# Optimization experiments

Hardware: AMD Instinct MI355X
Metric: run time of the kernel (lower is better)

The kernel has to match this reference:

```python
import jax, jax.numpy as jnp
import numpy as np

N, E, D, H1, H2 = 50000, 800000, 128, 128, 128


def setup_inputs() -> dict:
    key = jax.random.key(0)
    ks = jax.random.split(key, 9)
    s = 0.05
    return {
        "x": jax.random.normal(ks[0], (N, D), dtype=jnp.float32),
        "edge_index": jax.random.randint(ks[1], (2, E), 0, N, dtype=jnp.int64),
        "W_l1": jax.random.normal(ks[2], (D, H1), dtype=jnp.float32) * s,
        "b_l1": jnp.zeros((H1,), dtype=jnp.float32),
        "W_r1": jax.random.normal(ks[3], (D, H1), dtype=jnp.float32) * s,
        "W_l2": jax.random.normal(ks[4], (H1, H2), dtype=jnp.float32) * s,
        "b_l2": jnp.zeros((H2,), dtype=jnp.float32),
        "W_r2": jax.random.normal(ks[5], (H1, H2), dtype=jnp.float32) * s,
        "W_e": jax.random.normal(ks[6], (2 * H2, 1), dtype=jnp.float32) * s,
        "b_e": jnp.zeros((1,), dtype=jnp.float32),
    }


def _sage_conv(h, src, tgt, n_nodes, W_l, b_l, W_r):
    # PyG SAGEConv (mean aggr): out = lin_l(mean_{j in N(i)} h_j) + lin_r(h_i)
    msg = h[src]                                              # [E, F] gather
    agg = jax.ops.segment_sum(msg, tgt, num_segments=n_nodes)  # [N, F]
    cnt = jax.ops.segment_sum(jnp.ones((src.shape[0], 1), h.dtype), tgt,
                              num_segments=n_nodes)            # [N, 1]
    mean = agg / jnp.maximum(cnt, 1.0)                         # empty nbrs -> 0
    return mean @ W_l + b_l + h @ W_r


def reference(x, edge_index, W_l1, b_l1, W_r1, W_l2, b_l2, W_r2, W_e, b_e):
    src, tgt = edge_index[0], edge_index[1]
    n_nodes = x.shape[0]
    h = jax.nn.relu(_sage_conv(x, src, tgt, n_nodes, W_l1, b_l1, W_r1))
    # dropout is identity in eval mode
    h = _sage_conv(h, src, tgt, n_nodes, W_l2, b_l2, W_r2)
    z = jnp.concatenate([h[src], h[tgt]], axis=-1)  # [E, 2*H2]
    y = z @ W_e + b_e                                # [E, 1]
    return jax.nn.sigmoid(y)
```

## Files before the change

### kernel.cpp

```cpp
#include <hip/hip_runtime.h>

#define NN 50000
#define NE 800000
#define DD 128
#define BUCKETS 196
#define PB 4096
#define PBLK 196
#define EMAX 6144
#define PACKB 6250
#define WTB 128

typedef unsigned int uint_t;
typedef unsigned short ush_t;
typedef __attribute__((ext_vector_type(8))) short short8;
typedef __attribute__((ext_vector_type(4))) float f32x4;

__device__ __forceinline__ float bflo(uint_t u) { return __uint_as_float(u << 16); }
__device__ __forceinline__ float bfhi(uint_t u) { return __uint_as_float(u & 0xffff0000u); }
__device__ __forceinline__ ush_t f2bf(float f) {
  uint_t u = __float_as_uint(f);
  u += 0x7fffu + ((u >> 16) & 1u);
  return (ush_t)(u >> 16);
}
__device__ __forceinline__ uint_t pack2(float a, float b) {
  return (uint_t)f2bf(a) | ((uint_t)f2bf(b) << 16);
}

__device__ __forceinline__ int ld_idx(const void* ei, int is64, long long i) {
  return is64 ? (int)((const long long*)ei)[i] : ((const int*)ei)[i];
}

__device__ __forceinline__ int detect64(const void* ei) {
  const unsigned long long* p = (const unsigned long long*)ei;
  unsigned long long w = p[threadIdx.x & 63];
  return __ballot((w >> 32) != 0) == 0ull ? 1 : 0;
}

__device__ __forceinline__ int block_incl_scan(int v, int tid, int* wsum) {
  int lane = tid & 63, wave = tid >> 6;
  int s = v;
#pragma unroll
  for (int off = 1; off < 64; off <<= 1) {
    int u = __shfl_up(s, off, 64);
    if (lane >= off) s += u;
  }
  if (lane == 63) wsum[wave] = s;
  __syncthreads();
  int base = 0;
  if (wave > 0) base += wsum[0];
  if (wave > 1) base += wsum[1];
  if (wave > 2) base += wsum[2];
  return base + s;
}

__global__ __launch_bounds__(256) void prep_part_k(
    const void* __restrict__ ei, int* __restrict__ bcur,
    uint_t* __restrict__ pbuf, uint_t* __restrict__ epk,
    const float* __restrict__ x, ush_t* __restrict__ xb,
    const float* __restrict__ Wl1, const float* __restrict__ Wr1,
    const float* __restrict__ Wl2, const float* __restrict__ Wr2,
    const float* __restrict__ We, const float* __restrict__ bl2,
    const float* __restrict__ be,
    ush_t* __restrict__ Wt1, float* __restrict__ uv, float* __restrict__ cc) {
  __shared__ int hist[256];
  __shared__ int basel[256];
  __shared__ int cur[256];
  __shared__ int gbase[256];
  __shared__ int wsum[4];
  __shared__ uint_t buf[PB];
  __shared__ unsigned char bbuf[PB];
  int tid = threadIdx.x;
  int blk = blockIdx.x;
  if (blk >= PBLK) {
    int blk2 = blk - PBLK;
    if (blk2 < 2) {
      const float* W = blk2 ? Wr2 : Wl2;
      int base = blk2 * 256;
      int wave = tid >> 6, lane = tid & 63;
      float e0 = We[lane], e1 = We[64 + lane];
      float f0 = We[128 + lane], f1 = We[192 + lane];
      for (int k = wave * 32; k < wave * 32 + 32; ++k) {
        float m0 = W[k * DD + lane];
        float m1 = W[k * DD + 64 + lane];
        float p = m0 * e0 + m1 * e1;
        float q = m0 * f0 + m1 * f1;
#pragma unroll
        for (int off = 32; off > 0; off >>= 1) {
          p += __shfl_down(p, off, 64);
          q += __shfl_down(q, off, 64);
        }
        if (lane == 0) {
          uv[base + k] = p;
          uv[base + 128 + k] = q;
        }
      }
      return;
    }
    if (blk2 == 2) {
      if (tid < 64) {
        int k = tid;
        float p = bl2[k] * (We[k] + We[128 + k]) +
                  bl2[k + 64] * (We[k + 64] + We[192 + k]);
#pragma unroll
        for (int off = 32; off > 0; off >>= 1) p += __shfl_down(p, off, 64);
        if (k == 0) cc[0] = p + be[0];
      }
      return;
    }
    blk2 -= 3;
    if (blk2 < PACKB) {
      int i = blk2 * 256 + tid;
      float4 v = reinterpret_cast<const float4*>(x)[i];
      uint2 o;
      o.x = pack2(v.x, v.y);
      o.y = pack2(v.z, v.w);
      reinterpret_cast<uint2*>(xb)[i] = o;
      return;
    }
    blk2 -= PACKB;
    int e = blk2 * 256 + tid;
    int col = e >> 8;
    int k = e & 255;
    float v = (k < DD) ? Wl1[k * DD + col] : Wr1[(k - DD) * DD + col];
    Wt1[col * 256 + k] = f2bf(v);
    return;
  }
  int is64 = detect64(ei);
  hist[tid] = 0;
  __syncthreads();
  long long base = (long long)blk * PB;
  uint_t pv[PB / 256];
#pragma unroll
  for (int i = 0; i < PB / 256; ++i) {
    long long e = base + i * 256 + tid;
    if (e < NE) {
      int s = ld_idx(ei, is64, e);
      int d = ld_idx(ei, is64, (long long)NE + e);
      pv[i] = ((uint_t)(d >> 8) << 24) | ((uint_t)(d & 255) << 16) | (uint_t)s;
      epk[e] = ((uint_t)d << 16) | (uint_t)s;
      atomicAdd(&hist[d >> 8], 1);
    } else {
      pv[i] = 0xFFFFFFFFu;
    }
  }
  __syncthreads();
  int hv = hist[tid];
  int incl = block_incl_scan(hv, tid, wsum);
  basel[tid] = incl - hv;
  cur[tid] = incl - hv;
  if (hv > 0) gbase[tid] = atomicAdd(&bcur[tid], hv);
  __syncthreads();
#pragma unroll
  for (int i = 0; i < PB / 256; ++i) {
    uint_t p = pv[i];
    if (p != 0xFFFFFFFFu) {
      int b = p >> 24;
      int r = atomicAdd(&cur[b], 1);
      buf[r] = p & 0xFFFFFFu;
      bbuf[r] = (unsigned char)b;
    }
  }
  __syncthreads();
  int total = basel[255] + hist[255];
  for (int j = tid; j < total; j += 256) {
    int b = bbuf[j];
    int slot = gbase[b] + (j - basel[b]);
    if (slot < EMAX) pbuf[(size_t)b * EMAX + slot] = buf[j];
  }
}

__global__ __launch_bounds__(256) void csr_k(const uint_t* __restrict__ pbuf,
                                             const int* __restrict__ bcur,
                                             int* __restrict__ offsets,
                                             int* __restrict__ srclist) {
  __shared__ int cnt[256];
  __shared__ int scur[256];
  __shared__ int wsum[4];
  __shared__ int sgb, scnt, stot;
  __shared__ uint_t ebuf[EMAX];
  int tid = threadIdx.x;
  int b = blockIdx.x;
  int v = 0;
  if (tid < BUCKETS) {
    v = bcur[tid];
    if (v > EMAX) v = EMAX;
  }
  int incl = block_incl_scan(v, tid, wsum);
  if (tid == b) { sgb = incl - v; scnt = v; }
  if (tid == BUCKETS - 1) stot = incl;
  cnt[tid] = 0;
  __syncthreads();
  int gb = sgb;
  int ecnt = scnt;
  for (int j = tid; j < ecnt; j += 256) {
    uint_t e = pbuf[(size_t)b * EMAX + j];
    ebuf[j] = e;
    atomicAdd(&cnt[(e >> 16) & 255], 1);
  }
  __syncthreads();
  int c = cnt[tid];
  int incl2 = block_incl_scan(c, tid, wsum);
  int ex = incl2 - c;
  scur[tid] = ex;
  int node = b * 256 + tid;
  if (node < NN) offsets[node] = gb + ex;
  if (b == BUCKETS - 1 && tid == 0) offsets[NN] = stot;
  __syncthreads();
  for (int j = tid; j < ecnt; j += 256) {
    uint_t e = ebuf[j];
    int p = atomicAdd(&scur[(e >> 16) & 255], 1);
    srclist[gb + p] = (int)(e & 0xFFFFu);
  }
}

__global__ __launch_bounds__(256, 2) void agg_l1_k(
    const ush_t* __restrict__ xb, const int* __restrict__ srclist,
    const int* __restrict__ offsets, const ush_t* __restrict__ Wt1,
    const float* __restrict__ bl, const float* __restrict__ uv,
    float2* __restrict__ t12, float2* __restrict__ r12) {
  __shared__ ush_t sB[128 * 256];
  __shared__ ush_t sM[64 * 128];
  int tid = threadIdx.x;
  int lane = tid & 63;
  int wave = tid >> 6;
  int n15 = lane & 15, quad = lane >> 4;
  int nb = blockIdx.x * 64;

#pragma unroll
  for (int it = 0; it < 16; ++it) {
    int i = it * 256 + tid;
    int col = i >> 5, c2 = i & 31;
    int byt = (col << 9) + (c2 << 4);
    byt ^= (col & 7) << 4;
    *reinterpret_cast<short8*>(reinterpret_cast<char*>(sB) + byt) =
        reinterpret_cast<const short8*>(Wt1)[i];
  }

  int g = tid >> 4, lane16 = tid & 15;
  int f = lane16 << 3;
  for (int p = 0; p < 4; ++p) {
    int lr = p * 16 + g;
    int node = nb + lr;
    float a0 = 0.f, a1 = 0.f, a2 = 0.f, a3 = 0.f;
    float a4 = 0.f, a5 = 0.f, a6 = 0.f, a7 = 0.f;
    int beg = 0, end = 0;
    if (node < NN) {
      beg = offsets[node];
      end = offsets[node + 1];
    }
    for (int c = beg; c < end; c += 16) {
      int idx = c + lane16;
      int sl = (idx < end) ? srclist[idx] : 0;
      int m = min(16, end - c);
      int jj = 0;
      for (; jj + 4 <= m; jj += 4) {
        int s0 = __shfl(sl, jj, 16);
        int s1 = __shfl(sl, jj + 1, 16);
        int s2 = __shfl(sl, jj + 2, 16);
        int s3 = __shfl(sl, jj + 3, 16);
        uint4 v0 = *reinterpret_cast<const uint4*>(xb + (size_t)s0 * DD + f);
        uint4 v1 = *reinterpret_cast<const uint4*>(xb + (size_t)s1 * DD + f);
        uint4 v2 = *reinterpret_cast<const uint4*>(xb + (size_t)s2 * DD + f);
        uint4 v3 = *reinterpret_cast<const uint4*>(xb + (size_t)s3 * DD + f);
        a0 += bflo(v0.x); a1 += bfhi(v0.x); a2 += bflo(v0.y); a3 += bfhi(v0.y);
        a4 += bflo(v0.z); a5 += bfhi(v0.z); a6 += bflo(v0.w); a7 += bfhi(v0.w);
        a0 += bflo(v1.x); a1 += bfhi(v1.x); a2 += bflo(v1.y); a3 += bfhi(v1.y);
        a4 += bflo(v1.z); a5 += bfhi(v1.z); a6 += bflo(v1.w); a7 += bfhi(v1.w);
        a0 += bflo(v2.x); a1 += bfhi(v2.x); a2 += bflo(v2.y); a3 += bfhi(v2.y);
        a4 += bflo(v2.z); a5 += bfhi(v2.z); a6 += bflo(v2.w); a7 += bfhi(v2.w);
        a0 += bflo(v3.x); a1 += bfhi(v3.x); a2 += bflo(v3.y); a3 += bfhi(v3.y);
        a4 += bflo(v3.z); a5 += bfhi(v3.z); a6 += bflo(v3.w); a7 += bfhi(v3.w);
      }
      for (; jj < m; ++jj) {
        int s = __shfl(sl, jj, 16);
        uint4 v = *reinterpret_cast<const uint4*>(xb + (size_t)s * DD + f);
        a0 += bflo(v.x); a1 += bfhi(v.x); a2 += bflo(v.y); a3 += bfhi(v.y);
        a4 += bflo(v.z); a5 += bfhi(v.z); a6 += bflo(v.w); a7 += bfhi(v.w);
      }
    }
    float inv = 1.0f / fmaxf((float)(end - beg), 1.0f);
    uint4 o;
    o.x = pack2(a0 * inv, a1 * inv);
    o.y = pack2(a2 * inv, a3 * inv);
    o.z = pack2(a4 * inv, a5 * inv);
    o.w = pack2(a6 * inv, a7 * inv);
    int byt = (lr << 8) + (lane16 << 4);
    byt ^= (lr & 7) << 4;
    *reinterpret_cast<uint4*>(reinterpret_cast<char*>(sM) + byt) = o;
  }
  __syncthreads();

  int row = nb + wave * 16 + n15;
  int arow = (row < NN) ? row : (NN - 1);
  const ush_t* a1p = xb + (size_t)arow * DD;
  int lr = wave * 16 + n15;
  f32x4 acc[8];
#pragma unroll
  for (int t = 0; t < 8; ++t) acc[t] = (f32x4){0.f, 0.f, 0.f, 0.f};
#pragma unroll
  for (int c = 0; c < 8; ++c) {
    short8 af;
    if (c < 4) {
      int byt = (lr << 8) + (c << 6) + (quad << 4);
      byt ^= (lr & 7) << 4;
      af = *reinterpret_cast<const short8*>(reinterpret_cast<const char*>(sM) + byt);
    } else {
      af = *reinterpret_cast<const short8*>(a1p + (c - 4) * 32 + quad * 8);
    }
#pragma unroll
    for (int t = 0; t < 8; ++t) {
      int brow = t * 16 + n15;
      int byt = (brow << 9) + (c << 6) + (quad << 4);
      byt ^= (brow & 7) << 4;
      short8 bf = *reinterpret_cast<const short8*>(reinterpret_cast<const char*>(sB) + byt);
      acc[t] = __builtin_amdgcn_mfma_f32_16x16x32_bf16(af, bf, acc[t], 0, 0, 0);
    }
  }

  float p1[4] = {0.f, 0.f, 0.f, 0.f};
  float p2[4] = {0.f, 0.f, 0.f, 0.f};
  float q1[4] = {0.f, 0.f, 0.f, 0.f};
  float q2[4] = {0.f, 0.f, 0.f, 0.f};
#pragma unroll
  for (int t = 0; t < 8; ++t) {
    int col = t * 16 + n15;
    float b = bl[col];
    float U1 = uv[col];
    float U2 = uv[128 + col];
    float V1 = uv[256 + col];
    float V2 = uv[384 + col];
#pragma unroll
    for (int reg = 0; reg < 4; ++reg) {
      float h = fmaxf(acc[t][reg] + b, 0.f);
      p1[reg] += h * U1;
      p2[reg] += h * U2;
      q1[reg] += h * V1;
      q2[reg] += h * V2;
    }
  }
#pragma unroll
  for (int reg = 0; reg < 4; ++reg) {
    float a1 = p1[reg], a2 = p2[reg], b1 = q1[reg], b2 = q2[reg];
    for (int off = 8; off > 0; off >>= 1) {
      a1 += __shfl_down(a1, off, 16);
      a2 += __shfl_down(a2, off, 16);
      b1 += __shfl_down(b1, off, 16);
      b2 += __shfl_down(b2, off, 16);
    }
    int r = nb + wave * 16 + quad * 4 + reg;
    if (n15 == 0 && r < NN) {
      t12[r] = make_float2(a1, a2);
      r12[r] = make_float2(b1, b2);
    }
  }
}

__global__ __launch_bounds__(256) void agg2s_k(const float2* __restrict__ t12,
                                               const int* __restrict__ srclist,
                                               const int* __restrict__ offsets,
                                               const float2* __restrict__ r12,
                                               float2* __restrict__ s12) {
  int t = blockIdx.x * 256 + threadIdx.x;
  int node = t >> 4;
  int lane = t & 15;
  int beg = offsets[node];
  int end = offsets[node + 1];
  float sx = 0.f, sy = 0.f;
  for (int c = beg + lane; c < end; c += 16) {
    int s = srclist[c];
    float2 v = t12[s];
    sx += v.x;
    sy += v.y;
  }
  for (int off = 8; off > 0; off >>= 1) {
    sx += __shfl_down(sx, off, 16);
    sy += __shfl_down(sy, off, 16);
  }
  if (lane == 0) {
    float inv = 1.0f / fmaxf((float)(end - beg), 1.0f);
    float2 r = r12[node];
    s12[node] = make_float2(sx * inv + r.x, sy * inv + r.y);
  }
}

__global__ __launch_bounds__(256) void edge_k(const uint_t* __restrict__ epk,
                                              const float2* __restrict__ s12,
                                              const float* __restrict__ cc,
                                              float* __restrict__ out) {
  int e = blockIdx.x * 256 + threadIdx.x;
  uint_t p = epk[e];
  float2 a = s12[p & 0xFFFFu];
  float2 b = s12[p >> 16];
  float v = a.x + b.y + cc[0];
  out[e] = 1.0f / (1.0f + __expf(-v));
}

extern "C" void kernel_launch(void* const* d_in, const int* in_sizes, int n_in,
                              void* d_out, int out_size, void* d_ws, size_t ws_size,
                              hipStream_t stream) {
  const float* x   = (const float*)d_in[0];
  const void*  ei  = d_in[1];
  const float* Wl1 = (const float*)d_in[2];
  const float* bl1 = (const float*)d_in[3];
  const float* Wr1 = (const float*)d_in[4];
  const float* Wl2 = (const float*)d_in[5];
  const float* bl2 = (const float*)d_in[6];
  const float* Wr2 = (const float*)d_in[7];
  const float* We  = (const float*)d_in[8];
  const float* be  = (const float*)d_in[9];
  float* out = (float*)d_out;

  int* bcur    = (int*)d_ws;
  int* offsets = bcur + 256;
  uint_t* epk  = (uint_t*)(offsets + 50004);
  uint_t* pbuf = epk + NE;
  int* srclist = (int*)(pbuf + (size_t)BUCKETS * EMAX);
  ush_t* xb    = (ush_t*)(srclist + NE);
  float2* t12  = (float2*)(xb + (size_t)NN * DD);
  float2* r12  = t12 + NN;
  float2* s12  = r12 + NN;
  ush_t* Wt1   = (ush_t*)(s12 + NN);
  float* uv    = (float*)(Wt1 + 32768);
  float* cc    = uv + 512;

  hipMemsetAsync(bcur, 0, 256 * sizeof(int), stream);
  prep_part_k<<<PBLK + 3 + PACKB + WTB, 256, 0, stream>>>(
      ei, bcur, pbuf, epk, x, xb, Wl1, Wr1, Wl2, Wr2, We, bl2, be, Wt1, uv, cc);
  csr_k<<<BUCKETS, 256, 0, stream>>>(pbuf, bcur, offsets, srclist);

  int gemm_blocks = (NN + 63) / 64;
  agg_l1_k<<<gemm_blocks, 256, 0, stream>>>(xb, srclist, offsets, Wt1, bl1, uv,
                                            t12, r12);

  agg2s_k<<<(NN * 16) / 256, 256, 0, stream>>>(t12, srclist, offsets, r12, s12);

  edge_k<<<NE / 256, 256, 0, stream>>>(epk, s12, cc, out);
}
```

Before: 191.0 us.

## Split layer-1 aggregation into chunked-feature gather kernel and separate MFMA GEMM

Stores the bf16 copy of x in a feature-chunked layout (8 chunks of 16 features per node), so each gather block touches only a 6.4 MB slice that can stay cache resident. A new agg_k kernel computes the neighbour means per chunk and writes them to global memory. A separate sage_l1 kernel then runs the MFMA GEMM, reading A rows from global memory and B from a padded shared layout instead of the XOR swizzle. srclist also shrinks to 16-bit indices. This adds an extra global round trip of the mean matrix and one more launch in exchange for better cache locality in the gather.

```diff
diff --git a/kernel.cpp b/kernel.cpp
--- a/kernel.cpp
+++ b/kernel.cpp
@@ -7,7 +7,8 @@
 #define PB 4096
 #define PBLK 196
 #define EMAX 6144
-#define PACKB 6250
+#define BPAD 264
+#define PACKB 3125
 #define WTB 128
 
 typedef unsigned int uint_t;
@@ -56,7 +57,7 @@
 __global__ __launch_bounds__(256) void prep_part_k(
     const void* __restrict__ ei, int* __restrict__ bcur,
     uint_t* __restrict__ pbuf, uint_t* __restrict__ epk,
-    const float* __restrict__ x, ush_t* __restrict__ xb,
+    const float* __restrict__ x, ush_t* __restrict__ xbc,
     const float* __restrict__ Wl1, const float* __restrict__ Wr1,
     const float* __restrict__ Wl2, const float* __restrict__ Wr2,
     const float* __restrict__ We, const float* __restrict__ bl2,
@@ -110,11 +111,19 @@
     blk2 -= 3;
     if (blk2 < PACKB) {
       int i = blk2 * 256 + tid;
-      float4 v = reinterpret_cast<const float4*>(x)[i];
-      uint2 o;
-      o.x = pack2(v.x, v.y);
-      o.y = pack2(v.z, v.w);
-      reinterpret_cast<uint2*>(xb)[i] = o;
+      int node = i >> 4;
+      int g = i & 15;
+      const float4* xp = reinterpret_cast<const float4*>(x) + (size_t)i * 2;
+      float4 v0 = xp[0];
+      float4 v1 = xp[1];
+      uint4 o;
+      o.x = pack2(v0.x, v0.y);
+      o.y = pack2(v0.z, v0.w);
+      o.z = pack2(v1.x, v1.y);
+      o.w = pack2(v1.z, v1.w);
+      int chunk = g >> 1;
+      int l8 = (g & 1) * 8;
+      *reinterpret_cast<uint4*>(xbc + ((size_t)chunk * NN + node) * 16 + l8) = o;
       return;
     }
     blk2 -= PACKB;
@@ -172,7 +181,7 @@
 __global__ __launch_bounds__(256) void csr_k(const uint_t* __restrict__ pbuf,
                                              const int* __restrict__ bcur,
                                              int* __restrict__ offsets,
-                                             int* __restrict__ srclist) {
+                                             ush_t* __restrict__ srclist) {
   __shared__ int cnt[256];
   __shared__ int scur[256];
   __shared__ int wsum[4];
@@ -209,91 +218,82 @@
   for (int j = tid; j < ecnt; j += 256) {
     uint_t e = ebuf[j];
     int p = atomicAdd(&scur[(e >> 16) & 255], 1);
-    srclist[gb + p] = (int)(e & 0xFFFFu);
-  }
-}
-
-__global__ __launch_bounds__(256, 2) void agg_l1_k(
-    const ush_t* __restrict__ xb, const int* __restrict__ srclist,
-    const int* __restrict__ offsets, const ush_t* __restrict__ Wt1,
-    const float* __restrict__ bl, const float* __restrict__ uv,
-    float2* __restrict__ t12, float2* __restrict__ r12) {
-  __shared__ ush_t sB[128 * 256];
-  __shared__ ush_t sM[64 * 128];
+    srclist[gb + p] = (ush_t)(e & 0xFFFFu);
+  }
+}
+
+__global__ __launch_bounds__(256) void agg_k(const ush_t* __restrict__ xbc,
+                                             const ush_t* __restrict__ srclist,
+                                             const int* __restrict__ offsets,
+                                             ush_t* __restrict__ meanb) {
+  int bid = blockIdx.x;
+  int chunk = bid & 7;
+  int grp = bid >> 3;
+  int tid = threadIdx.x;
+  int node = grp * 128 + (tid >> 1);
+  if (node >= NN) return;
+  int half = tid & 1;
+  const ush_t* base = xbc + (size_t)chunk * NN * 16 + half * 8;
+  int beg = offsets[node];
+  int end = offsets[node + 1];
+  float a0 = 0.f, a1 = 0.f, a2 = 0.f, a3 = 0.f;
+  float a4 = 0.f, a5 = 0.f, a6 = 0.f, a7 = 0.f;
+  int e = beg;
+  for (; e + 4 <= end; e += 4) {
+    int s0 = srclist[e];
+    int s1 = srclist[e + 1];
+    int s2 = srclist[e + 2];
+    int s3 = srclist[e + 3];
+    uint4 v0 = *reinterpret_cast<const uint4*>(base + (size_t)s0 * 16);
+    uint4 v1 = *reinterpret_cast<const uint4*>(base + (size_t)s1 * 16);
+    uint4 v2 = *reinterpret_cast<const uint4*>(base + (size_t)s2 * 16);
+    uint4 v3 = *reinterpret_cast<const uint4*>(base + (size_t)s3 * 16);
+    a0 += bflo(v0.x); a1 += bfhi(v0.x); a2 += bflo(v0.y); a3 += bfhi(v0.y);
+    a4 += bflo(v0.z); a5 += bfhi(v0.z); a6 += bflo(v0.w); a7 += bfhi(v0.w);
+    a0 += bflo(v1.x); a1 += bfhi(v1.x); a2 += bflo(v1.y); a3 += bfhi(v1.y);
+    a4 += bflo(v1.z); a5 += bfhi(v1.z); a6 += bflo(v1.w); a7 += bfhi(v1.w);
+    a0 += bflo(v2.x); a1 += bfhi(v2.x); a2 += bflo(v2.y); a3 += bfhi(v2.y);
+    a4 += bflo(v2.z); a5 += bfhi(v2.z); a6 += bflo(v2.w); a7 += bfhi(v2.w);
+    a0 += bflo(v3.x); a1 += bfhi(v3.x); a2 += bflo(v3.y); a3 += bfhi(v3.y);
+    a4 += bflo(v3.z); a5 += bfhi(v3.z); a6 += bflo(v3.w); a7 += bfhi(v3.w);
+  }
+  for (; e < end; ++e) {
+    int s = srclist[e];
+    uint4 v = *reinterpret_cast<const uint4*>(base + (size_t)s * 16);
+    a0 += bflo(v.x); a1 += bfhi(v.x); a2 += bflo(v.y); a3 += bfhi(v.y);
+    a4 += bflo(v.z); a5 += bfhi(v.z); a6 += bflo(v.w); a7 += bfhi(v.w);
+  }
+  float inv = 1.0f / fmaxf((float)(end - beg), 1.0f);
+  uint4 o;
+  o.x = pack2(a0 * inv, a1 * inv);
+  o.y = pack2(a2 * inv, a3 * inv);
+  o.z = pack2(a4 * inv, a5 * inv);
+  o.w = pack2(a6 * inv, a7 * inv);
+  *reinterpret_cast<uint4*>(meanb + (size_t)node * DD + chunk * 16 + half * 8) = o;
+}
+
+__global__ __launch_bounds__(256, 2) void sage_l1(
+    const ush_t* __restrict__ meanb, const ush_t* __restrict__ xbc,
+    const ush_t* __restrict__ Wt1, const float* __restrict__ bl,
+    const float* __restrict__ uv, float2* __restrict__ t12,
+    float2* __restrict__ r12) {
+  __shared__ ush_t sB[128 * BPAD];
   int tid = threadIdx.x;
   int lane = tid & 63;
   int wave = tid >> 6;
   int n15 = lane & 15, quad = lane >> 4;
   int nb = blockIdx.x * 64;
-
 #pragma unroll
   for (int it = 0; it < 16; ++it) {
     int i = it * 256 + tid;
-    int col = i >> 5, c2 = i & 31;
-    int byt = (col << 9) + (c2 << 4);
-    byt ^= (col & 7) << 4;
-    *reinterpret_cast<short8*>(reinterpret_cast<char*>(sB) + byt) =
+    int col = i >> 5, c = i & 31;
+    *reinterpret_cast<short8*>(&sB[col * BPAD + c * 8]) =
         reinterpret_cast<const short8*>(Wt1)[i];
   }
-
-  int g = tid >> 4, lane16 = tid & 15;
-  int f = lane16 << 3;
-  for (int p = 0; p < 4; ++p) {
-    int lr = p * 16 + g;
-    int node = nb + lr;
-    float a0 = 0.f, a1 = 0.f, a2 = 0.f, a3 = 0.f;
-    float a4 = 0.f, a5 = 0.f, a6 = 0.f, a7 = 0.f;
-    int beg = 0, end = 0;
-    if (node < NN) {
-      beg = offsets[node];
-      end = offsets[node + 1];
-    }
-    for (int c = beg; c < end; c += 16) {
-      int idx = c + lane16;
-      int sl = (idx < end) ? srclist[idx] : 0;
-      int m = min(16, end - c);
-      int jj = 0;
-      for (; jj + 4 <= m; jj += 4) {
-        int s0 = __shfl(sl, jj, 16);
-        int s1 = __shfl(sl, jj + 1, 16);
-        int s2 = __shfl(sl, jj + 2, 16);
-        int s3 = __shfl(sl, jj + 3, 16);
-        uint4 v0 = *reinterpret_cast<const uint4*>(xb + (size_t)s0 * DD + f);
-        uint4 v1 = *reinterpret_cast<const uint4*>(xb + (size_t)s1 * DD + f);
-        uint4 v2 = *reinterpret_cast<const uint4*>(xb + (size_t)s2 * DD + f);
-        uint4 v3 = *reinterpret_cast<const uint4*>(xb + (size_t)s3 * DD + f);
-        a0 += bflo(v0.x); a1 += bfhi(v0.x); a2 += bflo(v0.y); a3 += bfhi(v0.y);
-        a4 += bflo(v0.z); a5 += bfhi(v0.z); a6 += bflo(v0.w); a7 += bfhi(v0.w);
-        a0 += bflo(v1.x); a1 += bfhi(v1.x); a2 += bflo(v1.y); a3 += bfhi(v1.y);
-        a4 += bflo(v1.z); a5 += bfhi(v1.z); a6 += bflo(v1.w); a7 += bfhi(v1.w);
-        a0 += bflo(v2.x); a1 += bfhi(v2.x); a2 += bflo(v2.y); a3 += bfhi(v2.y);
-        a4 += bflo(v2.z); a5 += bfhi(v2.z); a6 += bflo(v2.w); a7 += bfhi(v2.w);
-        a0 += bflo(v3.x); a1 += bfhi(v3.x); a2 += bflo(v3.y); a3 += bfhi(v3.y);
-        a4 += bflo(v3.z); a5 += bfhi(v3.z); a6 += bflo(v3.w); a7 += bfhi(v3.w);
-      }
-      for (; jj < m; ++jj) {
-        int s = __shfl(sl, jj, 16);
-        uint4 v = *reinterpret_cast<const uint4*>(xb + (size_t)s * DD + f);
-        a0 += bflo(v.x); a1 += bfhi(v.x); a2 += bflo(v.y); a3 += bfhi(v.y);
-        a4 += bflo(v.z); a5 += bfhi(v.z); a6 += bflo(v.w); a7 += bfhi(v.w);
-      }
-    }
-    float inv = 1.0f / fmaxf((float)(end - beg), 1.0f);
-    uint4 o;
-    o.x = pack2(a0 * inv, a1 * inv);
-    o.y = pack2(a2 * inv, a3 * inv);
-    o.z = pack2(a4 * inv, a5 * inv);
-    o.w = pack2(a6 * inv, a7 * inv);
-    int byt = (lr << 8) + (lane16 << 4);
-    byt ^= (lr & 7) << 4;
-    *reinterpret_cast<uint4*>(reinterpret_cast<char*>(sM) + byt) = o;
-  }
-  __syncthreads();
-
+  __syncthreads();
   int row = nb + wave * 16 + n15;
   int arow = (row < NN) ? row : (NN - 1);
-  const ush_t* a1p = xb + (size_t)arow * DD;
-  int lr = wave * 16 + n15;
+  const ush_t* a0 = meanb + (size_t)arow * DD;
   f32x4 acc[8];
 #pragma unroll
   for (int t = 0; t < 8; ++t) acc[t] = (f32x4){0.f, 0.f, 0.f, 0.f};
@@ -301,22 +301,19 @@
   for (int c = 0; c < 8; ++c) {
     short8 af;
     if (c < 4) {
-      int byt = (lr << 8) + (c << 6) + (quad << 4);
-      byt ^= (lr & 7) << 4;
-      af = *reinterpret_cast<const short8*>(reinterpret_cast<const char*>(sM) + byt);
+      af = *reinterpret_cast<const short8*>(a0 + c * 32 + quad * 8);
     } else {
-      af = *reinterpret_cast<const short8*>(a1p + (c - 4) * 32 + quad * 8);
-    }
+      int fb = (c - 4) * 32 + quad * 8;
+      af = *reinterpret_cast<const short8*>(
+          xbc + ((size_t)(fb >> 4) * NN + arow) * 16 + (fb & 15));
+    }
+    int kb = c * 32 + quad * 8;
 #pragma unroll
     for (int t = 0; t < 8; ++t) {
-      int brow = t * 16 + n15;
-      int byt = (brow << 9) + (c << 6) + (quad << 4);
-      byt ^= (brow & 7) << 4;
-      short8 bf = *reinterpret_cast<const short8*>(reinterpret_cast<const char*>(sB) + byt);
+      short8 bf = *reinterpret_cast<const short8*>(&sB[(t * 16 + n15) * BPAD + kb]);
       acc[t] = __builtin_amdgcn_mfma_f32_16x16x32_bf16(af, bf, acc[t], 0, 0, 0);
     }
   }
-
   float p1[4] = {0.f, 0.f, 0.f, 0.f};
   float p2[4] = {0.f, 0.f, 0.f, 0.f};
   float q1[4] = {0.f, 0.f, 0.f, 0.f};
@@ -356,7 +353,7 @@
 }
 
 __global__ __launch_bounds__(256) void agg2s_k(const float2* __restrict__ t12,
-                                               const int* __restrict__ srclist,
+                                               const ush_t* __restrict__ srclist,
                                                const int* __restrict__ offsets,
                                                const float2* __restrict__ r12,
                                                float2* __restrict__ s12) {
@@ -410,27 +407,28 @@
   const float* be  = (const float*)d_in[9];
   float* out = (float*)d_out;
 
-  int* bcur    = (int*)d_ws;
-  int* offsets = bcur + 256;
-  uint_t* epk  = (uint_t*)(offsets + 50004);
-  uint_t* pbuf = epk + NE;
-  int* srclist = (int*)(pbuf + (size_t)BUCKETS * EMAX);
-  ush_t* xb    = (ush_t*)(srclist + NE);
-  float2* t12  = (float2*)(xb + (size_t)NN * DD);
-  float2* r12  = t12 + NN;
-  float2* s12  = r12 + NN;
-  ush_t* Wt1   = (ush_t*)(s12 + NN);
-  float* uv    = (float*)(Wt1 + 32768);
-  float* cc    = uv + 512;
+  int* bcur       = (int*)d_ws;
+  int* offsets    = bcur + 256;
+  uint_t* epk     = (uint_t*)(offsets + 50004);
+  uint_t* pbuf    = epk + NE;
+  ush_t* srclist  = (ush_t*)(pbuf + (size_t)BUCKETS * EMAX);
+  ush_t* xbc      = srclist + NE;
+  ush_t* meanb    = xbc + (size_t)NN * DD;
+  float2* t12     = (float2*)(meanb + (size_t)NN * DD);
+  float2* r12     = t12 + NN;
+  float2* s12     = r12 + NN;
+  ush_t* Wt1      = (ush_t*)(s12 + NN);
+  float* uv       = (float*)(Wt1 + 32768);
+  float* cc       = uv + 512;
 
   hipMemsetAsync(bcur, 0, 256 * sizeof(int), stream);
   prep_part_k<<<PBLK + 3 + PACKB + WTB, 256, 0, stream>>>(
-      ei, bcur, pbuf, epk, x, xb, Wl1, Wr1, Wl2, Wr2, We, bl2, be, Wt1, uv, cc);
+      ei, bcur, pbuf, epk, x, xbc, Wl1, Wr1, Wl2, Wr2, We, bl2, be, Wt1, uv, cc);
   csr_k<<<BUCKETS, 256, 0, stream>>>(pbuf, bcur, offsets, srclist);
 
-  int gemm_blocks = (NN + 63) / 64;
-  agg_l1_k<<<gemm_blocks, 256, 0, stream>>>(xb, srclist, offsets, Wt1, bl1, uv,
-                                            t12, r12);
+  agg_k<<<((NN + 127) / 128) * 8, 256, 0, stream>>>(xbc, srclist, offsets, meanb);
+
+  sage_l1<<<(NN + 63) / 64, 256, 0, stream>>>(meanb, xbc, Wt1, bl1, uv, t12, r12);
 
   agg2s_k<<<(NN * 16) / 256, 256, 0, stream>>>(t12, srclist, offsets, r12, s12);
 
```

Result: no change. 190.9 us (-0.1%).
